# Optimization experiments

Hardware: AMD Instinct MI355X
Metric: run time of the kernel (lower is better)

Reference implementation:

```python
import jax, jax.numpy as jnp
import numpy as np

N = 8192
IN_DIM = 128
HID = 32


def setup_inputs() -> dict:
    key = jax.random.key(0)
    ks = jax.random.split(key, 8)
    x = jax.random.normal(ks[0], (N, IN_DIM), dtype=jnp.float32)
    adj = jax.random.uniform(ks[1], (N, N), dtype=jnp.float32)
    # Linear params (torch nn.Linear: y = x @ W.T + b); store as [in, out] for einsum.
    def lin(k, fan_in, fan_out):
        bound = 1.0 / np.sqrt(fan_in)
        kw, kb = jax.random.split(k)
        W = jax.random.uniform(kw, (fan_in, fan_out), minval=-bound, maxval=bound, dtype=jnp.float32)
        b = jax.random.uniform(kb, (fan_out,), minval=-bound, maxval=bound, dtype=jnp.float32)
        return W, b
    W1, b1 = lin(ks[2], IN_DIM, HID)
    W2, b2 = lin(ks[3], HID, HID)
    W3, b3 = lin(ks[4], HID, 1)
    return {"x": x, "adj": adj, "W1": W1, "b1": b1, "W2": W2, "b2": b2, "W3": W3, "b3": b3}


def reference(x, adj, W1, b1, W2, b2, W3, b3):
    # a_hat = adj + I (self loops)
    n = adj.shape[0]
    a_hat = adj + jnp.eye(n, dtype=adj.dtype)
    degree = jnp.sum(a_hat, axis=1)
    d_inv_sqrt = jnp.clip(degree, 1.0, None) ** -0.5  # [N]
    # D^-1/2 A D^-1/2 as row/col scaling (same math as diag matmuls, no O(N^3) waste)
    a_norm = d_inv_sqrt[:, None] * a_hat * d_inv_sqrt[None, :]
    h = jax.nn.relu(a_norm @ (x @ W1 + b1))
    h = jax.nn.relu(a_norm @ (h @ W2 + b2))
    logits = (h @ W3 + b3).squeeze(-1)  # [N]
    return logits
```

## Files before the change

### kernel.cpp

```cpp
#include <hip/hip_runtime.h>
#include <math.h>

#define N 8192
#define IN_DIM 128
#define HID 32

#define RB 128
#define KT 64
#define SK 16
#define KCHUNK (N / SK)

__device__ __forceinline__ void fma4(float4& acc, float a, const float4& b) {
    acc.x = fmaf(a, b.x, acc.x);
    acc.y = fmaf(a, b.y, acc.y);
    acc.z = fmaf(a, b.z, acc.z);
    acc.w = fmaf(a, b.w, acc.w);
}

__global__ __launch_bounds__(256) void k_degree(const float* __restrict__ adj,
                                                float* __restrict__ dinv) {
    int row = blockIdx.x;
    const float4* rp = (const float4*)(adj + (size_t)row * N);
    int t = threadIdx.x;
    float s = 0.f;
#pragma unroll
    for (int i = 0; i < 8; ++i) {
        float4 v = rp[t + i * 256];
        s += v.x + v.y + v.z + v.w;
    }
    for (int off = 32; off > 0; off >>= 1) s += __shfl_down(s, off, 64);
    __shared__ float red[4];
    if ((t & 63) == 0) red[t >> 6] = s;
    __syncthreads();
    if (t == 0) {
        float deg = red[0] + red[1] + red[2] + red[3] + 1.0f;
        deg = fmaxf(deg, 1.0f);
        dinv[row] = 1.0f / sqrtf(deg);
    }
}

__global__ __launch_bounds__(256) void k_z1(const float* __restrict__ x,
                                            const float* __restrict__ W1,
                                            const float* __restrict__ b1,
                                            const float* __restrict__ dinv,
                                            float* __restrict__ Zs) {
    __shared__ float Ws[IN_DIM * HID];
    __shared__ float xs[8 * IN_DIM];
    int t = threadIdx.x;
    int row0 = blockIdx.x * 8;
#pragma unroll
    for (int i = 0; i < 4; ++i)
        *(float4*)&Ws[(i * 256 + t) * 4] = *(const float4*)&W1[(i * 256 + t) * 4];
    *(float4*)&xs[t * 4] = *(const float4*)&x[(size_t)row0 * IN_DIM + t * 4];
    __syncthreads();
    int r = t >> 5, c = t & 31;
    float acc = b1[c];
#pragma unroll 8
    for (int k = 0; k < IN_DIM; ++k) acc = fmaf(xs[r * IN_DIM + k], Ws[k * HID + c], acc);
    int row = row0 + r;
    Zs[(size_t)row * HID + c] = dinv[row] * acc;
}

__global__ __launch_bounds__(256) void k_spmm(const float* __restrict__ adj,
                                              const float* __restrict__ Zs,
                                              float* __restrict__ P) {
    __shared__ float As[RB * KT];
    __shared__ float Bs[KT][HID];
    int t = threadIdx.x;
    int r0 = blockIdx.x * RB;
    int k0 = blockIdx.y * KCHUNK;
    int cg = t & 3;
    int rp2 = (t >> 2) * 2;
    int e = (rp2 >> 1) & 7;
    float4 acc00 = {0, 0, 0, 0}, acc01 = {0, 0, 0, 0};
    float4 acc10 = {0, 0, 0, 0}, acc11 = {0, 0, 0, 0};

    for (int kt = k0; kt < k0 + KCHUNK; kt += KT) {
#pragma unroll
        for (int i = 0; i < 8; ++i) {
            int f = i * 256 + t;
            int row = f >> 4;
            int fi = f & 15;
            int sfi = fi ^ ((row >> 1) & 7);
            *(float4*)&As[row * KT + sfi * 4] =
                *(const float4*)&adj[(size_t)(r0 + row) * N + kt + fi * 4];
        }
#pragma unroll
        for (int i = 0; i < 2; ++i) {
            int f = i * 256 + t;
            ((float4*)&Bs[0][0])[f] = ((const float4*)(Zs + (size_t)kt * HID))[f];
        }
        __syncthreads();
#pragma unroll
        for (int kk = 0; kk < KT; kk += 4) {
            int s0 = ((kk >> 2) ^ e) * 4;
            float a0[4], a1[4];
            *(float4*)a0 = *(const float4*)&As[rp2 * KT + s0];
            *(float4*)a1 = *(const float4*)&As[(rp2 + 1) * KT + s0];
#pragma unroll
            for (int j = 0; j < 4; ++j) {
                float4 z0 = *(const float4*)&Bs[kk + j][cg * 8];
                float4 z1 = *(const float4*)&Bs[kk + j][cg * 8 + 4];
                fma4(acc00, a0[j], z0);
                fma4(acc01, a0[j], z1);
                fma4(acc10, a1[j], z0);
                fma4(acc11, a1[j], z1);
            }
        }
        __syncthreads();
    }

    float* p0 = P + (size_t)blockIdx.y * (N * HID) + (size_t)(r0 + rp2) * HID + cg * 8;
    float* p1 = p0 + HID;
    *(float4*)(p0)     = acc00;
    *(float4*)(p0 + 4) = acc01;
    *(float4*)(p1)     = acc10;
    *(float4*)(p1 + 4) = acc11;
}

__global__ __launch_bounds__(256) void k_fin_z2(const float* __restrict__ P,
                                                const float* __restrict__ Zin,
                                                const float* __restrict__ dinv,
                                                const float* __restrict__ W2,
                                                const float* __restrict__ b2,
                                                float* __restrict__ Zout) {
    __shared__ float Ws[HID * HID];
    __shared__ float hs[8][HID];
    int t = threadIdx.x;
    int row0 = blockIdx.x * 8;
    *(float4*)&Ws[t * 4] = *(const float4*)&W2[t * 4];
    int r = t >> 5, c = t & 31;
    size_t idx = (size_t)row0 * HID + t;
    float v = Zin[idx];
#pragma unroll
    for (int s = 0; s < SK; ++s) v += P[(size_t)s * (N * HID) + idx];
    int row = row0 + r;
    hs[r][c] = fmaxf(dinv[row] * v, 0.f);
    __syncthreads();
    float acc = b2[c];
#pragma unroll
    for (int k = 0; k < HID; ++k) acc = fmaf(hs[r][k], Ws[k * HID + c], acc);
    Zout[idx] = dinv[row] * acc;
}

__global__ __launch_bounds__(256) void k_fin_out(const float* __restrict__ P,
                                                 const float* __restrict__ Zin,
                                                 const float* __restrict__ dinv,
                                                 const float* __restrict__ W3,
                                                 const float* __restrict__ b3,
                                                 float* __restrict__ out) {
    int t = threadIdx.x;
    size_t idx = (size_t)blockIdx.x * 256 + t;
    int row = (int)(idx >> 5);
    int c = t & 31;
    float v = Zin[idx];
#pragma unroll
    for (int s = 0; s < SK; ++s) v += P[(size_t)s * (N * HID) + idx];
    float h = fmaxf(dinv[row] * v, 0.f);
    float hw = h * W3[c];
#pragma unroll
    for (int off = 16; off > 0; off >>= 1) hw += __shfl_xor(hw, off, 32);
    if (c == 0) out[row] = hw + b3[0];
}

extern "C" void kernel_launch(void* const* d_in, const int* in_sizes, int n_in,
                              void* d_out, int out_size, void* d_ws, size_t ws_size,
                              hipStream_t stream) {
    const float* x   = (const float*)d_in[0];
    const float* adj = (const float*)d_in[1];
    const float* W1  = (const float*)d_in[2];
    const float* b1  = (const float*)d_in[3];
    const float* W2  = (const float*)d_in[4];
    const float* b2  = (const float*)d_in[5];
    const float* W3  = (const float*)d_in[6];
    const float* b3  = (const float*)d_in[7];
    float* out = (float*)d_out;

    float* dinv = (float*)d_ws;
    float* Zs1  = dinv + N;
    float* Zs2  = Zs1 + (size_t)N * HID;
    float* P    = Zs2 + (size_t)N * HID;

    k_degree<<<N, 256, 0, stream>>>(adj, dinv);
    k_z1<<<N / 8, 256, 0, stream>>>(x, W1, b1, dinv, Zs1);

    k_spmm<<<dim3(N / RB, SK), 256, 0, stream>>>(adj, Zs1, P);
    k_fin_z2<<<N / 8, 256, 0, stream>>>(P, Zs1, dinv, W2, b2, Zs2);

    k_spmm<<<dim3(N / RB, SK), 256, 0, stream>>>(adj, Zs2, P);
    k_fin_out<<<N * HID / 256, 256, 0, stream>>>(P, Zs2, dinv, W3, b3, out);
}
```

Before: 522.8 us.

## Rewrite spmm to stream adjacency rows directly per thread without LDS tiling

The dense adj@Z kernel drops shared-memory staging and barriers. Each thread now owns two full rows and accumulates all 32 output columns in registers, reading adj with float4 loads straight from global memory and Z as wave-uniform broadcast loads. The K dimension is split 64 ways instead of 16. The aim is to remove LDS traffic and sync overhead. In exchange, per-thread adj loads are strided by row, so coalescing is poor. P also grows 4x, and k_fin_z2/k_fin_out still sum only SK slices, which now matches the new SK but means more work in the finalize kernels.

Result: slower. 758.5 us (+45.1%).

```diff
diff --git a/kernel.cpp b/kernel.cpp
--- a/kernel.cpp
+++ b/kernel.cpp
@@ -5,9 +5,9 @@
 #define IN_DIM 128
 #define HID 32
 
-#define RB 128
-#define KT 64
-#define SK 16
+#define RBW 128
+#define RB 512
+#define SK 64
 #define KCHUNK (N / SK)
 
 __device__ __forceinline__ void fma4(float4& acc, float a, const float4& b) {
@@ -61,61 +61,43 @@
     Zs[(size_t)row * HID + c] = dinv[row] * acc;
 }
 
-__global__ __launch_bounds__(256) void k_spmm(const float* __restrict__ adj,
-                                              const float* __restrict__ Zs,
-                                              float* __restrict__ P) {
-    __shared__ float As[RB * KT];
-    __shared__ float Bs[KT][HID];
+__global__ __launch_bounds__(256, 4) void k_spmm(const float* __restrict__ adj,
+                                                 const float* __restrict__ Zs,
+                                                 float* __restrict__ P) {
     int t = threadIdx.x;
-    int r0 = blockIdx.x * RB;
-    int k0 = blockIdx.y * KCHUNK;
-    int cg = t & 3;
-    int rp2 = (t >> 2) * 2;
-    int e = (rp2 >> 1) & 7;
-    float4 acc00 = {0, 0, 0, 0}, acc01 = {0, 0, 0, 0};
-    float4 acc10 = {0, 0, 0, 0}, acc11 = {0, 0, 0, 0};
+    int w = t >> 6, l = t & 63;
+    int row = blockIdx.x * RB + w * RBW + l * 2;
+    int kbeg = blockIdx.y * KCHUNK;
+    const float* a0 = adj + (size_t)row * N;
+    const float* a1 = a0 + N;
+    float4 acc0[8] = {{0,0,0,0},{0,0,0,0},{0,0,0,0},{0,0,0,0},
+                      {0,0,0,0},{0,0,0,0},{0,0,0,0},{0,0,0,0}};
+    float4 acc1[8] = {{0,0,0,0},{0,0,0,0},{0,0,0,0},{0,0,0,0},
+                      {0,0,0,0},{0,0,0,0},{0,0,0,0},{0,0,0,0}};
 
-    for (int kt = k0; kt < k0 + KCHUNK; kt += KT) {
+#pragma unroll 2
+    for (int k = kbeg; k < kbeg + KCHUNK; k += 4) {
+        float4 A0 = *(const float4*)&a0[k];
+        float4 A1 = *(const float4*)&a1[k];
+        const float* B = Zs + (size_t)k * HID;
+        float a0j[4] = {A0.x, A0.y, A0.z, A0.w};
+        float a1j[4] = {A1.x, A1.y, A1.z, A1.w};
 #pragma unroll
-        for (int i = 0; i < 8; ++i) {
-            int f = i * 256 + t;
-            int row = f >> 4;
-            int fi = f & 15;
-            int sfi = fi ^ ((row >> 1) & 7);
-            *(float4*)&As[row * KT + sfi * 4] =
-                *(const float4*)&adj[(size_t)(r0 + row) * N + kt + fi * 4];
-        }
+        for (int j = 0; j < 4; ++j) {
 #pragma unroll
-        for (int i = 0; i < 2; ++i) {
-            int f = i * 256 + t;
-            ((float4*)&Bs[0][0])[f] = ((const float4*)(Zs + (size_t)kt * HID))[f];
-        }
-        __syncthreads();
-#pragma unroll
-        for (int kk = 0; kk < KT; kk += 4) {
-            int s0 = ((kk >> 2) ^ e) * 4;
-            float a0[4], a1[4];
-            *(float4*)a0 = *(const float4*)&As[rp2 * KT + s0];
-            *(float4*)a1 = *(const float4*)&As[(rp2 + 1) * KT + s0];
-#pragma unroll
-            for (int j = 0; j < 4; ++j) {
-                float4 z0 = *(const float4*)&Bs[kk + j][cg * 8];
-                float4 z1 = *(const float4*)&Bs[kk + j][cg * 8 + 4];
-                fma4(acc00, a0[j], z0);
-                fma4(acc01, a0[j], z1);
-                fma4(acc10, a1[j], z0);
-                fma4(acc11, a1[j], z1);
+            for (int cc = 0; cc < 8; ++cc) {
+                float4 b = *(const float4*)&B[j * HID + cc * 4];
+                fma4(acc0[cc], a0j[j], b);
+                fma4(acc1[cc], a1j[j], b);
             }
         }
-        __syncthreads();
     }
 
-    float* p0 = P + (size_t)blockIdx.y * (N * HID) + (size_t)(r0 + rp2) * HID + cg * 8;
-    float* p1 = p0 + HID;
-    *(float4*)(p0)     = acc00;
-    *(float4*)(p0 + 4) = acc01;
-    *(float4*)(p1)     = acc10;
-    *(float4*)(p1 + 4) = acc11;
+    float* p0 = P + (size_t)blockIdx.y * (N * HID) + (size_t)row * HID;
+#pragma unroll
+    for (int cc = 0; cc < 8; ++cc) *(float4*)&p0[cc * 4] = acc0[cc];
+#pragma unroll
+    for (int cc = 0; cc < 8; ++cc) *(float4*)&p0[HID + cc * 4] = acc1[cc];
 }
 
 __global__ __launch_bounds__(256) void k_fin_z2(const float* __restrict__ P,
```
